# Optimization experiments

Measured on AMD Instinct MI355X. Metric: run time of the kernel, lower is better.

## Reference

```python
import jax, jax.numpy as jnp
import numpy as np

# OGB/PyG molecular featurization vocab sizes (x_map / e_map)
NODE_VOCABS = [119, 9, 11, 12, 10, 5, 8, 2, 2]   # 9 atom features
EDGE_VOCABS = [22, 6, 2]                          # 3 bond features
HID, OUT, LAYERS = 128, 256, 3
N_NODES, N_EDGES, N_GRAPHS = 200000, 400000, 8000
NODE_OFF = np.concatenate([[0], np.cumsum(NODE_VOCABS)[:-1]]).astype(np.int32)
EDGE_OFF = np.concatenate([[0], np.cumsum(EDGE_VOCABS)[:-1]]).astype(np.int32)
NODE_TOT = int(np.sum(NODE_VOCABS))
EDGE_TOT = int(np.sum(EDGE_VOCABS))


def setup_inputs() -> dict:
    key = jax.random.key(0)
    ks = jax.random.split(key, 16)
    # integer graph data (values in-range per categorical column via modulo)
    x = jax.random.randint(ks[0], (N_NODES, 9), 0, 1 << 30) % jnp.asarray(NODE_VOCABS)
    edge_attr = jax.random.randint(ks[1], (N_EDGES, 3), 0, 1 << 30) % jnp.asarray(EDGE_VOCABS)
    edge_index = jax.random.randint(ks[2], (2, N_EDGES), 0, N_NODES)
    batch = jnp.sort(jax.random.randint(ks[3], (N_NODES,), 0, N_GRAPHS))
    s = 0.02
    return {
        "x": x, "edge_attr": edge_attr, "edge_index": edge_index, "batch": batch,
        # embedding tables packed row-wise with per-feature offsets
        "node_emb": jax.random.normal(ks[4], (NODE_TOT, HID), jnp.float32) * s,
        "edge_emb": jax.random.normal(ks[5], (EDGE_TOT, HID), jnp.float32) * s,
        "node_proj_w": jax.random.normal(ks[6], (9 * HID, HID), jnp.float32) * s,
        "node_proj_b": jnp.zeros((HID,), jnp.float32),
        "edge_proj_w": jax.random.normal(ks[7], (3 * HID, HID), jnp.float32) * s,
        "edge_proj_b": jnp.zeros((HID,), jnp.float32),
        "mlp_w1": jax.random.normal(ks[8], (LAYERS, HID, HID), jnp.float32) * s,
        "mlp_b1": jnp.zeros((LAYERS, HID), jnp.float32),
        "mlp_w2": jax.random.normal(ks[9], (LAYERS, HID, HID), jnp.float32) * s,
        "mlp_b2": jnp.zeros((LAYERS, HID), jnp.float32),
        "proj_w": jax.random.normal(ks[10], (HID, OUT), jnp.float32) * s,
        "proj_b": jnp.zeros((OUT,), jnp.float32),
    }


def reference(x, edge_attr, edge_index, batch,
              node_emb, edge_emb,
              node_proj_w, node_proj_b, edge_proj_w, edge_proj_b,
              mlp_w1, mlp_b1, mlp_w2, mlp_b2, proj_w, proj_b):
    n = x.shape[0]
    e = edge_attr.shape[0]
    # embedding lookup per categorical column, concat, project -> [N, HID]
    nf = node_emb[x + jnp.asarray(NODE_OFF)].reshape(n, 9 * HID)
    h = nf @ node_proj_w + node_proj_b
    ef = edge_emb[edge_attr + jnp.asarray(EDGE_OFF)].reshape(e, 3 * HID)
    ef = ef @ edge_proj_w + edge_proj_b
    src, dst = edge_index[0], edge_index[1]
    for l in range(LAYERS):
        # GINEConv (eps=0): mlp(x + sum_{j->i} relu(x_j + e_ji)), then outer relu
        m = jax.nn.relu(h[src] + ef)                       # [E, HID] gather + fuse
        agg = jax.ops.segment_sum(m, dst, num_segments=N_NODES)
        z = h + agg
        z = jax.nn.relu(z @ mlp_w1[l] + mlp_b1[l]) @ mlp_w2[l] + mlp_b2[l]
        h = jax.nn.relu(z)
    g = jax.ops.segment_sum(h, batch, num_segments=N_GRAPHS)  # global_add_pool
    p = g @ proj_w + proj_b
    norm = jnp.maximum(jnp.linalg.norm(p, axis=-1, keepdims=True), 1e-12)
    return p / norm
```

## Files before the change

kernel.cpp:

```cpp
#include <hip/hip_runtime.h>
#include <hip/hip_bf16.h>

#define NN 200000
#define NE 400000
#define NG 8000
#define HID 128
#define OUTD 256
#define NODE_TOT 178
#define EDGE_TOT 30
#define NCOMBO 264
#define SCAN_NB 196

typedef __attribute__((ext_vector_type(8))) short bfrag8;
typedef __attribute__((ext_vector_type(4))) short bfrag4;
typedef __attribute__((ext_vector_type(4))) float f32x4;
typedef unsigned short ushort_t;

__constant__ int c_noff[10] = {0,119,128,139,151,161,166,174,176,178};

__device__ __forceinline__ ushort_t f2bf(float f) {
  union { float f; unsigned u; } x; x.f = f;
  unsigned r = x.u + 0x7fffu + ((x.u >> 16) & 1u);
  return (ushort_t)(r >> 16);
}
__device__ __forceinline__ float bf2f(ushort_t u) {
  union { unsigned u; float f; } x; x.u = ((unsigned)u) << 16;
  return x.f;
}

__global__ __launch_bounds__(128) void build_tables(
    const float* __restrict__ node_emb, const float* __restrict__ edge_emb,
    const float* __restrict__ npw, const float* __restrict__ npb,
    const float* __restrict__ epw, const float* __restrict__ epb,
    float* __restrict__ PN, float* __restrict__ PE)
{
  int r = blockIdx.x, d = threadIdx.x;
  if (r < NODE_TOT) {
    int c = 0;
    while (r >= c_noff[c+1]) c++;
    float acc = (c == 0) ? npb[d] : 0.f;
    const float* er = node_emb + r*HID;
    const float* wb = npw + (size_t)(c*HID)*HID + d;
    for (int k = 0; k < HID; k++) acc += er[k] * wb[(size_t)k*HID];
    PN[r*HID + d] = acc;
  } else {
    int re = r - NODE_TOT;
    int c = (re >= 28) ? 2 : (re >= 22 ? 1 : 0);
    float acc = (c == 0) ? epb[d] : 0.f;
    const float* er = edge_emb + re*HID;
    const float* wb = epw + (size_t)(c*HID)*HID + d;
    for (int k = 0; k < HID; k++) acc += er[k] * wb[(size_t)k*HID];
    PE[re*HID + d] = acc;
  }
}

__global__ __launch_bounds__(64) void build_pe3(const float* __restrict__ PE,
                                                unsigned* __restrict__ pe3b)
{
  int c = blockIdx.x, lane = threadIdx.x;
  int a2 = c & 1, a1 = (c >> 1) % 6, a0 = (c >> 1) / 6;
  int d = lane*2;
  float v0 = PE[a0*HID + d]   + PE[(22+a1)*HID + d]   + PE[(28+a2)*HID + d];
  float v1 = PE[a0*HID + d+1] + PE[(22+a1)*HID + d+1] + PE[(28+a2)*HID + d+1];
  pe3b[c*64 + lane] = (unsigned)f2bf(v0) | ((unsigned)f2bf(v1) << 16);
}

__global__ __launch_bounds__(256) void pack_w1(const float* __restrict__ w1,
                                               ushort_t* __restrict__ pw)
{
  int t = blockIdx.x*256 + threadIdx.x;
  int lane = t & 63, tile = (t >> 6) & 31, layer = t >> 11;
  int nt = tile >> 2, kt = tile & 3;
  int n  = nt*16 + (lane & 15);
  int k0 = kt*32 + ((lane >> 4) << 3);
  const float* src = w1 + (size_t)layer*HID*HID;
  ushort_t* dst = pw + (size_t)layer*32768 + (size_t)tile*512 + lane*8;
  #pragma unroll
  for (int j = 0; j < 8; j++) dst[j] = f2bf(src[(size_t)(k0+j)*HID + n]);
}

__global__ __launch_bounds__(256) void pack_w2(const float* __restrict__ w2,
                                               ushort_t* __restrict__ pw)
{
  int t = blockIdx.x*256 + threadIdx.x;
  int lane = t & 63, frag = (t >> 6) & 63, layer = t >> 12;
  int it = frag >> 3, kk = frag & 7;
  int i  = it*16 + (lane & 15);
  int k0 = kk*16 + ((lane >> 4) << 2);
  const float* src = w2 + (size_t)layer*HID*HID;
  ushort_t* dst = pw + (size_t)layer*32768 + 16384 + (size_t)frag*256 + lane*4;
  #pragma unroll
  for (int j = 0; j < 4; j++) dst[j] = f2bf(src[(size_t)(k0+j)*HID + i]);
}

__global__ __launch_bounds__(256) void node_embed(const int* __restrict__ x,
                                                  const float* __restrict__ PN,
                                                  ushort_t* __restrict__ h)
{
  int gid = blockIdx.x*256 + threadIdx.x;
  int i = gid >> 5, d0 = (gid & 31) << 2;
  const int* xr = x + i*9;
  f32x4 acc = {0.f, 0.f, 0.f, 0.f};
  #pragma unroll
  for (int c = 0; c < 9; c++)
    acc += *(const f32x4*)&PN[(c_noff[c] + xr[c])*HID + d0];
  uint2 pk;
  pk.x = (unsigned)f2bf(acc[0]) | ((unsigned)f2bf(acc[1]) << 16);
  pk.y = (unsigned)f2bf(acc[2]) | ((unsigned)f2bf(acc[3]) << 16);
  *(uint2*)&h[(size_t)i*HID + d0] = pk;
}

__global__ __launch_bounds__(256) void hist(const int* __restrict__ ei, int* __restrict__ deg) {
  int e = blockIdx.x*256 + threadIdx.x;
  if (e < NE) atomicAdd(&deg[ei[NE + e]], 1);
}

__global__ __launch_bounds__(256) void scan1(const int* __restrict__ deg,
                                             int* __restrict__ rowptr,
                                             int* __restrict__ bsum)
{
  __shared__ int sd[256];
  int b = blockIdx.x, t = threadIdx.x;
  int idx0 = b*1024 + t*4;
  int v[4]; int s = 0;
  #pragma unroll
  for (int j = 0; j < 4; j++) { int i = idx0 + j; v[j] = (i < NN) ? deg[i] : 0; s += v[j]; }
  sd[t] = s; __syncthreads();
  for (int off = 1; off < 256; off <<= 1) {
    int x = (t >= off) ? sd[t - off] : 0; __syncthreads();
    sd[t] += x; __syncthreads();
  }
  int run = (t > 0) ? sd[t-1] : 0;
  #pragma unroll
  for (int j = 0; j < 4; j++) { int i = idx0 + j; run += v[j]; if (i < NN) rowptr[i+1] = run; }
  if (t == 255) bsum[b] = sd[255];
}

__global__ __launch_bounds__(256) void scan2(int* __restrict__ bsum) {
  __shared__ int sd[256];
  int t = threadIdx.x;
  sd[t] = (t < SCAN_NB) ? bsum[t] : 0; __syncthreads();
  for (int off = 1; off < 256; off <<= 1) {
    int x = (t >= off) ? sd[t - off] : 0; __syncthreads();
    sd[t] += x; __syncthreads();
  }
  if (t < SCAN_NB) bsum[t] = sd[t];
}

__global__ __launch_bounds__(256) void scan3(int* __restrict__ rowptr, const int* __restrict__ bsum) {
  int b = blockIdx.x, t = threadIdx.x;
  if (b == 0) { if (t == 0) rowptr[0] = 0; return; }
  int add = bsum[b-1];
  int idx0 = b*1024 + t*4;
  #pragma unroll
  for (int j = 0; j < 4; j++) { int i = idx0 + j; if (i < NN) rowptr[i+1] += add; }
}

__global__ __launch_bounds__(256) void scatter_e(const int* __restrict__ ei,
                                                 const int* __restrict__ ea,
                                                 int* __restrict__ cursor,
                                                 unsigned* __restrict__ elist,
                                                 unsigned char* __restrict__ dloc)
{
  int e = blockIdx.x*256 + threadIdx.x;
  if (e >= NE) return;
  int src = ei[e], dst = ei[NE + e];
  const int* ar = ea + e*3;
  unsigned combo = (unsigned)((ar[0]*6 + ar[1])*2 + ar[2]);
  int pos = atomicAdd(&cursor[dst], 1);
  elist[pos] = (unsigned)src | (combo << 18);
  dloc[pos] = (unsigned char)(dst & 63);
}

__global__ __launch_bounds__(256) void gine_layer(
    const ushort_t* __restrict__ hin, ushort_t* __restrict__ hout,
    const int* __restrict__ rowptr, const unsigned* __restrict__ elist,
    const unsigned char* __restrict__ dloc,
    const unsigned* __restrict__ pe3b,
    const ushort_t* __restrict__ pw,
    const float* __restrict__ b1, const float* __restrict__ b2)
{
  __shared__ ushort_t aggs[64*136];
  int tid = threadIdx.x;
  int w = tid >> 6, lane = tid & 63;
  int q = lane >> 4;
  int rb = blockIdx.x*64 + w*16;
  const unsigned* h2 = (const unsigned*)hin;

  #pragma unroll
  for (int r = 0; r < 16; r++)
    ((unsigned*)&aggs[(w*16 + r)*136])[lane] = 0;

  int s = rowptr[rb], E = rowptr[rb + 16];
  int cur = -1;
  float ax = 0.f, ay = 0.f;

  auto proc = [&](int dl, unsigned hv, unsigned tt) {
    int dlu = __builtin_amdgcn_readfirstlane(dl);
    if (dlu != cur) {
      if (cur >= 0)
        ((unsigned*)&aggs[cur*136])[lane] =
            (unsigned)f2bf(ax) | ((unsigned)f2bf(ay) << 16);
      cur = dlu; ax = 0.f; ay = 0.f;
    }
    ax += fmaxf(bf2f((ushort_t)(hv & 0xffff)) + bf2f((ushort_t)(tt & 0xffff)), 0.f);
    ay += fmaxf(bf2f((ushort_t)(hv >> 16)) + bf2f((ushort_t)(tt >> 16)), 0.f);
  };

  int j = s;
  for (; j + 3 < E; j += 4) {
    unsigned pk0 = elist[j],   pk1 = elist[j+1];
    unsigned pk2 = elist[j+2], pk3 = elist[j+3];
    int d0 = dloc[j],   d1 = dloc[j+1];
    int d2 = dloc[j+2], d3 = dloc[j+3];
    unsigned hv0 = h2[(size_t)(pk0 & 0x3ffff)*64 + lane];
    unsigned hv1 = h2[(size_t)(pk1 & 0x3ffff)*64 + lane];
    unsigned hv2 = h2[(size_t)(pk2 & 0x3ffff)*64 + lane];
    unsigned hv3 = h2[(size_t)(pk3 & 0x3ffff)*64 + lane];
    unsigned t0 = pe3b[(pk0 >> 18)*64 + lane];
    unsigned t1 = pe3b[(pk1 >> 18)*64 + lane];
    unsigned t2 = pe3b[(pk2 >> 18)*64 + lane];
    unsigned t3 = pe3b[(pk3 >> 18)*64 + lane];
    proc(d0, hv0, t0); proc(d1, hv1, t1);
    proc(d2, hv2, t2); proc(d3, hv3, t3);
  }
  for (; j < E; ++j) {
    unsigned pk = elist[j];
    int dl = dloc[j];
    unsigned hv = h2[(size_t)(pk & 0x3ffff)*64 + lane];
    unsigned tt = pe3b[(pk >> 18)*64 + lane];
    proc(dl, hv, tt);
  }
  if (cur >= 0)
    ((unsigned*)&aggs[cur*136])[lane] =
        (unsigned)f2bf(ax) | ((unsigned)f2bf(ay) << 16);

  int n = rb + (lane & 15);
  int acol = q << 3;

  bfrag8 afr[4];
  #pragma unroll
  for (int kt = 0; kt < 4; kt++) {
    int c = kt*32 + acol;
    bfrag8 hfr = *(const bfrag8*)(hin + (size_t)n*HID + c);
    bfrag8 gfr = *(const bfrag8*)&aggs[(w*16 + (lane & 15))*136 + c];
    bfrag8 fr;
    #pragma unroll
    for (int j2 = 0; j2 < 8; j2++)
      fr[j2] = (short)f2bf(bf2f((ushort_t)hfr[j2]) + bf2f((ushort_t)gfr[j2]));
    afr[kt] = fr;
  }

  const bfrag8* w1f = (const bfrag8*)pw;
  const bfrag4* w2f = (const bfrag4*)(pw + 16384);

  f32x4 acc1[8];
  #pragma unroll
  for (int nt = 0; nt < 8; nt++)
    acc1[nt] = *(const f32x4*)&b1[nt*16 + q*4];
  #pragma unroll
  for (int kt = 0; kt < 4; kt++)
    #pragma unroll
    for (int nt = 0; nt < 8; nt++)
      acc1[nt] = __builtin_amdgcn_mfma_f32_16x16x32_bf16(w1f[(nt*4+kt)*64 + lane], afr[kt], acc1[nt], 0, 0, 0);

  bfrag4 t4[8];
  #pragma unroll
  for (int kk = 0; kk < 8; kk++) {
    bfrag4 v;
    #pragma unroll
    for (int r = 0; r < 4; r++) v[r] = (short)f2bf(fmaxf(acc1[kk][r], 0.f));
    t4[kk] = v;
  }

  #pragma unroll
  for (int it = 0; it < 8; it++) {
    f32x4 acc2 = *(const f32x4*)&b2[it*16 + q*4];
    #pragma unroll
    for (int kk = 0; kk < 8; kk++)
      acc2 = __builtin_amdgcn_mfma_f32_16x16x16bf16_1k(w2f[(it*8+kk)*64 + lane], t4[kk], acc2, 0, 0, 0);
    uint2 pk;
    pk.x = (unsigned)f2bf(fmaxf(acc2[0], 0.f)) | ((unsigned)f2bf(fmaxf(acc2[1], 0.f)) << 16);
    pk.y = (unsigned)f2bf(fmaxf(acc2[2], 0.f)) | ((unsigned)f2bf(fmaxf(acc2[3], 0.f)) << 16);
    *(uint2*)&hout[(size_t)n*HID + it*16 + q*4] = pk;
  }
}

__device__ __forceinline__ int lowerb(const int* a, int n, int v) {
  int lo = 0, hi = n;
  while (lo < hi) { int m = (lo + hi) >> 1; if (a[m] < v) lo = m + 1; else hi = m; }
  return lo;
}

__global__ __launch_bounds__(128) void pool(const ushort_t* __restrict__ h,
                                            const int* __restrict__ batch,
                                            float* __restrict__ gf)
{
  int g = blockIdx.x, d = threadIdx.x;
  int s = lowerb(batch, NN, g), e = lowerb(batch, NN, g + 1);
  float acc = 0.f;
  for (int i = s; i < e; i++) acc += bf2f(h[(size_t)i*HID + d]);
  gf[g*HID + d] = acc;
}

__global__ __launch_bounds__(256) void final_proj(const float* __restrict__ gf,
                                                  const float* __restrict__ W,
                                                  const float* __restrict__ b,
                                                  float* __restrict__ out)
{
  __shared__ float gls[16*128];
  __shared__ float part[16][4];
  int tid = threadIdx.x;
  int gbase = blockIdx.x*16;
  for (int idx = tid; idx < 2048; idx += 256) gls[idx] = gf[(size_t)gbase*128 + idx];
  __syncthreads();
  float acc[16];
  #pragma unroll
  for (int g = 0; g < 16; g++) acc[g] = 0.f;
  for (int k = 0; k < 128; k++) {
    float wv = W[(size_t)k*256 + tid];
    #pragma unroll
    for (int g = 0; g < 16; g++) acc[g] += gls[g*128 + k] * wv;
  }
  float bj = b[tid];
  int wid = tid >> 6, lane = tid & 63;
  #pragma unroll
  for (int g = 0; g < 16; g++) {
    acc[g] += bj;
    float s = acc[g]*acc[g];
    #pragma unroll
    for (int off = 32; off > 0; off >>= 1) s += __shfl_xor(s, off, 64);
    if (lane == 0) part[g][wid] = s;
  }
  __syncthreads();
  #pragma unroll
  for (int g = 0; g < 16; g++) {
    float S = part[g][0] + part[g][1] + part[g][2] + part[g][3];
    float rn = 1.f / fmaxf(sqrtf(S), 1e-12f);
    out[(size_t)(gbase + g)*256 + tid] = acc[g]*rn;
  }
}

__global__ __launch_bounds__(256) void ws_diag(float* __restrict__ out, int n, float wsval) {
  int i = blockIdx.x*256 + threadIdx.x;
  if (i < n) out[i] = (i == 0) ? wsval : 0.f;
}

extern "C" void kernel_launch(void* const* d_in, const int* in_sizes, int n_in,
                              void* d_out, int out_size, void* d_ws, size_t ws_size,
                              hipStream_t stream)
{
  const int*   x     = (const int*)d_in[0];
  const int*   ea    = (const int*)d_in[1];
  const int*   ei    = (const int*)d_in[2];
  const int*   batch = (const int*)d_in[3];
  const float* nemb  = (const float*)d_in[4];
  const float* eemb  = (const float*)d_in[5];
  const float* npw   = (const float*)d_in[6];
  const float* npb   = (const float*)d_in[7];
  const float* epw   = (const float*)d_in[8];
  const float* epb   = (const float*)d_in[9];
  const float* w1    = (const float*)d_in[10];
  const float* b1    = (const float*)d_in[11];
  const float* w2    = (const float*)d_in[12];
  const float* b2    = (const float*)d_in[13];
  const float* pjw   = (const float*)d_in[14];
  const float* pjb   = (const float*)d_in[15];
  float* out = (float*)d_out;

  char* ws = (char*)d_ws;
  size_t off = 0;
  auto carve = [&](size_t bytes) -> char* {
    char* p = ws + off;
    off = (off + bytes + 255) & ~(size_t)255;
    return p;
  };
  float*    PN     = (float*)carve((size_t)NODE_TOT*HID*4);
  float*    PE     = (float*)carve((size_t)EDGE_TOT*HID*4);
  unsigned* PE3b   = (unsigned*)carve((size_t)NCOMBO*64*4);
  ushort_t* PW     = (ushort_t*)carve((size_t)3*32768*2);
  ushort_t* hA     = (ushort_t*)carve((size_t)NN*HID*2);
  ushort_t* hB     = (ushort_t*)carve((size_t)NN*HID*2);
  float*    gf     = (float*)carve((size_t)NG*HID*4);
  int*      deg    = (int*)carve((size_t)NN*4);
  int*      rowptr = (int*)carve((size_t)(NN+1)*4);
  int*      cursor = (int*)carve((size_t)NN*4);
  int*      bsum   = (int*)carve((size_t)SCAN_NB*4);
  unsigned* elist  = (unsigned*)carve((size_t)NE*4);
  unsigned char* dlc = (unsigned char*)carve((size_t)NE);

  if (off > ws_size) {
    ws_diag<<<(out_size + 255)/256, 256, 0, stream>>>(out, out_size, (float)ws_size);
    return;
  }

  build_tables<<<NODE_TOT + EDGE_TOT, 128, 0, stream>>>(nemb, eemb, npw, npb, epw, epb, PN, PE);
  build_pe3<<<NCOMBO, 64, 0, stream>>>(PE, PE3b);
  pack_w1<<<24, 256, 0, stream>>>(w1, PW);
  pack_w2<<<48, 256, 0, stream>>>(w2, PW);
  node_embed<<<(NN*32)/256, 256, 0, stream>>>(x, PN, hA);

  hipMemsetAsync(deg, 0, (size_t)NN*4, stream);
  hist<<<(NE + 255)/256, 256, 0, stream>>>(ei, deg);
  scan1<<<SCAN_NB, 256, 0, stream>>>(deg, rowptr, bsum);
  scan2<<<1, 256, 0, stream>>>(bsum);
  scan3<<<SCAN_NB, 256, 0, stream>>>(rowptr, bsum);
  hipMemcpyAsync(cursor, rowptr, (size_t)NN*4, hipMemcpyDeviceToDevice, stream);
  scatter_e<<<(NE + 255)/256, 256, 0, stream>>>(ei, ea, cursor, elist, dlc);

  ushort_t* cur = hA; ushort_t* nxt = hB;
  for (int l = 0; l < 3; l++) {
    gine_layer<<<NN/64, 256, 0, stream>>>(cur, nxt, rowptr, elist, dlc, PE3b,
                                          PW + (size_t)l*32768, b1 + l*HID, b2 + l*HID);
    ushort_t* t = cur; cur = nxt; nxt = t;
  }
  pool<<<NG, 128, 0, stream>>>(cur, batch, gf);
  final_proj<<<NG/16, 256, 0, stream>>>(gf, pjw, pjb, out);
}
```

Baseline: 505.3 us.

## Fuse global add pool into last GINE layer and widen edge gather unroll

The last GINE layer is templated so that it keeps its output rows in shared memory and reduces them straight into per-graph sums with atomicAdd, which removes the separate pool kernel and its binary searches plus the write and re-read of the final node features. gf is now zeroed with a memset. The edge gather loop is unrolled from 4 to 8 to keep more memory loads in flight, and launch bounds request 4 blocks per CU. The cost is float atomic contention on gf, a nondeterministic summation order, and higher register pressure from the wider unroll.

```diff
diff --git a/kernel.cpp b/kernel.cpp
--- a/kernel.cpp
+++ b/kernel.cpp
@@ -172,20 +172,25 @@
   dloc[pos] = (unsigned char)(dst & 63);
 }
 
-__global__ __launch_bounds__(256) void gine_layer(
+template<bool LAST>
+__global__ __launch_bounds__(256, 4) void gine_layer(
     const ushort_t* __restrict__ hin, ushort_t* __restrict__ hout,
     const int* __restrict__ rowptr, const unsigned* __restrict__ elist,
     const unsigned char* __restrict__ dloc,
     const unsigned* __restrict__ pe3b,
     const ushort_t* __restrict__ pw,
-    const float* __restrict__ b1, const float* __restrict__ b2)
+    const float* __restrict__ b1, const float* __restrict__ b2,
+    const int* __restrict__ batch, float* __restrict__ gf)
 {
   __shared__ ushort_t aggs[64*136];
+  __shared__ int bids[64];
   int tid = threadIdx.x;
   int w = tid >> 6, lane = tid & 63;
   int q = lane >> 4;
   int rb = blockIdx.x*64 + w*16;
   const unsigned* h2 = (const unsigned*)hin;
+
+  if (LAST && tid < 64) bids[tid] = batch[blockIdx.x*64 + tid];
 
   #pragma unroll
   for (int r = 0; r < 16; r++)
@@ -208,21 +213,17 @@
   };
 
   int j = s;
-  for (; j + 3 < E; j += 4) {
-    unsigned pk0 = elist[j],   pk1 = elist[j+1];
-    unsigned pk2 = elist[j+2], pk3 = elist[j+3];
-    int d0 = dloc[j],   d1 = dloc[j+1];
-    int d2 = dloc[j+2], d3 = dloc[j+3];
-    unsigned hv0 = h2[(size_t)(pk0 & 0x3ffff)*64 + lane];
-    unsigned hv1 = h2[(size_t)(pk1 & 0x3ffff)*64 + lane];
-    unsigned hv2 = h2[(size_t)(pk2 & 0x3ffff)*64 + lane];
-    unsigned hv3 = h2[(size_t)(pk3 & 0x3ffff)*64 + lane];
-    unsigned t0 = pe3b[(pk0 >> 18)*64 + lane];
-    unsigned t1 = pe3b[(pk1 >> 18)*64 + lane];
-    unsigned t2 = pe3b[(pk2 >> 18)*64 + lane];
-    unsigned t3 = pe3b[(pk3 >> 18)*64 + lane];
-    proc(d0, hv0, t0); proc(d1, hv1, t1);
-    proc(d2, hv2, t2); proc(d3, hv3, t3);
+  for (; j + 7 < E; j += 8) {
+    unsigned pk[8]; int dl[8]; unsigned hv[8], tt[8];
+    #pragma unroll
+    for (int k = 0; k < 8; k++) { pk[k] = elist[j+k]; dl[k] = dloc[j+k]; }
+    #pragma unroll
+    for (int k = 0; k < 8; k++) {
+      hv[k] = h2[(size_t)(pk[k] & 0x3ffff)*64 + lane];
+      tt[k] = pe3b[(pk[k] >> 18)*64 + lane];
+    }
+    #pragma unroll
+    for (int k = 0; k < 8; k++) proc(dl[k], hv[k], tt[k]);
   }
   for (; j < E; ++j) {
     unsigned pk = elist[j];
@@ -251,6 +252,8 @@
     afr[kt] = fr;
   }
 
+  if (LAST) __syncthreads();
+
   const bfrag8* w1f = (const bfrag8*)pw;
   const bfrag4* w2f = (const bfrag4*)(pw + 16384);
 
@@ -282,25 +285,29 @@
     uint2 pk;
     pk.x = (unsigned)f2bf(fmaxf(acc2[0], 0.f)) | ((unsigned)f2bf(fmaxf(acc2[1], 0.f)) << 16);
     pk.y = (unsigned)f2bf(fmaxf(acc2[2], 0.f)) | ((unsigned)f2bf(fmaxf(acc2[3], 0.f)) << 16);
-    *(uint2*)&hout[(size_t)n*HID + it*16 + q*4] = pk;
-  }
-}
-
-__device__ __forceinline__ int lowerb(const int* a, int n, int v) {
-  int lo = 0, hi = n;
-  while (lo < hi) { int m = (lo + hi) >> 1; if (a[m] < v) lo = m + 1; else hi = m; }
-  return lo;
-}
-
-__global__ __launch_bounds__(128) void pool(const ushort_t* __restrict__ h,
-                                            const int* __restrict__ batch,
-                                            float* __restrict__ gf)
-{
-  int g = blockIdx.x, d = threadIdx.x;
-  int s = lowerb(batch, NN, g), e = lowerb(batch, NN, g + 1);
-  float acc = 0.f;
-  for (int i = s; i < e; i++) acc += bf2f(h[(size_t)i*HID + d]);
-  gf[g*HID + d] = acc;
+    if (LAST) {
+      *(uint2*)&aggs[(w*16 + (lane & 15))*136 + it*16 + q*4] = pk;
+    } else {
+      *(uint2*)&hout[(size_t)n*HID + it*16 + q*4] = pk;
+    }
+  }
+
+  if (LAST) {
+    __syncthreads();
+    int d = tid & 127, rh = tid >> 7;
+    float acc = 0.f;
+    int curg = bids[rh*32];
+    for (int r = 0; r < 32; r++) {
+      int row = rh*32 + r;
+      int g = bids[row];
+      if (g != curg) {
+        atomicAdd(&gf[(size_t)curg*HID + d], acc);
+        acc = 0.f; curg = g;
+      }
+      acc += bf2f(aggs[row*136 + d]);
+    }
+    atomicAdd(&gf[(size_t)curg*HID + d], acc);
+  }
 }
 
 __global__ __launch_bounds__(256) void final_proj(const float* __restrict__ gf,
@@ -401,6 +408,7 @@
   node_embed<<<(NN*32)/256, 256, 0, stream>>>(x, PN, hA);
 
   hipMemsetAsync(deg, 0, (size_t)NN*4, stream);
+  hipMemsetAsync(gf, 0, (size_t)NG*HID*4, stream);
   hist<<<(NE + 255)/256, 256, 0, stream>>>(ei, deg);
   scan1<<<SCAN_NB, 256, 0, stream>>>(deg, rowptr, bsum);
   scan2<<<1, 256, 0, stream>>>(bsum);
@@ -408,12 +416,12 @@
   hipMemcpyAsync(cursor, rowptr, (size_t)NN*4, hipMemcpyDeviceToDevice, stream);
   scatter_e<<<(NE + 255)/256, 256, 0, stream>>>(ei, ea, cursor, elist, dlc);
 
-  ushort_t* cur = hA; ushort_t* nxt = hB;
-  for (int l = 0; l < 3; l++) {
-    gine_layer<<<NN/64, 256, 0, stream>>>(cur, nxt, rowptr, elist, dlc, PE3b,
-                                          PW + (size_t)l*32768, b1 + l*HID, b2 + l*HID);
-    ushort_t* t = cur; cur = nxt; nxt = t;
-  }
-  pool<<<NG, 128, 0, stream>>>(cur, batch, gf);
+  gine_layer<false><<<NN/64, 256, 0, stream>>>(hA, hB, rowptr, elist, dlc, PE3b,
+                                               PW, b1, b2, batch, gf);
+  gine_layer<false><<<NN/64, 256, 0, stream>>>(hB, hA, rowptr, elist, dlc, PE3b,
+                                               PW + 32768, b1 + HID, b2 + HID, batch, gf);
+  gine_layer<true><<<NN/64, 256, 0, stream>>>(hA, hB, rowptr, elist, dlc, PE3b,
+                                              PW + 65536, b1 + 2*HID, b2 + 2*HID, batch, gf);
+
   final_proj<<<NG/16, 256, 0, stream>>>(gf, pjw, pjb, out);
 }
```

After: 447.9 us. -11.4%, faster.
